# Performance work log

Measured on AMD Instinct MI355X. Metric: run time of the kernel, lower is better.

## Reference

```python
import jax, jax.numpy as jnp
import numpy as np

NEG_SLOPE = 0.2
EPS = 1e-16  # PyG softmax denominator epsilon


def _add_self_loops(src, dst, edge_attr, n):
    # PyG add_self_loops with fill_value='mean': loop edge_attr = mean of
    # incoming edge_attr per target node (0 if no incoming edges).
    cnt = jax.ops.segment_sum(jnp.ones(dst.shape, edge_attr.dtype), dst, n)
    mean_attr = jax.ops.segment_sum(edge_attr, dst, n) / jnp.maximum(cnt, 1.0)[:, None]
    loop = jnp.arange(n)
    return (jnp.concatenate([src, loop]),
            jnp.concatenate([dst, loop]),
            jnp.concatenate([edge_attr, mean_attr], axis=0))


def _gatv2(x, src, dst, eattr, Wl, bl, Wr, br, We, att, bc, n):
    # heads=1, concat=False
    xl = x @ Wl + bl                     # [N, H] source transform
    xr = x @ Wr + br                     # [N, H] target transform
    ee = eattr @ We                      # [E, H]
    m = jax.nn.leaky_relu(xl[src] + xr[dst] + ee, NEG_SLOPE)  # [E, H]
    e = m @ att                          # [E]
    emax = jax.ops.segment_max(e, dst, n)
    emax = jnp.where(jnp.isfinite(emax), emax, 0.0)
    a = jnp.exp(e - emax[dst])
    denom = jax.ops.segment_sum(a, dst, n)
    alpha = a / (denom[dst] + EPS)       # softmax over incoming edges
    out = jax.ops.segment_sum(alpha[:, None] * xl[src], dst, n)  # [N, H]
    return out + bc


def setup_inputs() -> dict:
    key = jax.random.key(0)
    N, E, F_IN, H, E_DIM, OUT = 100000, 1200000, 64, 64, 16, 1
    ks = jax.random.split(key, 20)
    d = {}
    d['x'] = jax.random.normal(ks[0], (N, F_IN), jnp.float32)
    d['edge_index'] = jax.random.randint(ks[1], (2, E), 0, N, jnp.int64)
    d['edge_attr'] = jax.random.normal(ks[2], (E, E_DIM), jnp.float32)
    d['batch'] = jnp.zeros((N,), jnp.int64)
    s = 0.1
    # layer 1: in=F_IN -> H
    d['Wl1'] = jax.random.normal(ks[3], (F_IN, H), jnp.float32) * s
    d['bl1'] = jnp.zeros((H,), jnp.float32)
    d['Wr1'] = jax.random.normal(ks[4], (F_IN, H), jnp.float32) * s
    d['br1'] = jnp.zeros((H,), jnp.float32)
    d['We1'] = jax.random.normal(ks[5], (E_DIM, H), jnp.float32) * s
    d['att1'] = jax.random.normal(ks[6], (H,), jnp.float32) * s
    d['bc1'] = jnp.zeros((H,), jnp.float32)
    # layer 2: H -> H
    d['Wl2'] = jax.random.normal(ks[7], (H, H), jnp.float32) * s
    d['bl2'] = jnp.zeros((H,), jnp.float32)
    d['Wr2'] = jax.random.normal(ks[8], (H, H), jnp.float32) * s
    d['br2'] = jnp.zeros((H,), jnp.float32)
    d['We2'] = jax.random.normal(ks[9], (E_DIM, H), jnp.float32) * s
    d['att2'] = jax.random.normal(ks[10], (H,), jnp.float32) * s
    d['bc2'] = jnp.zeros((H,), jnp.float32)
    # JK(cat) readout: 2*H -> OUT
    d['Wout'] = jax.random.normal(ks[11], (2 * H, OUT), jnp.float32) * s
    d['bout'] = jnp.zeros((OUT,), jnp.float32)
    return d


def reference(x, edge_index, edge_attr, batch,
              Wl1, bl1, Wr1, br1, We1, att1, bc1,
              Wl2, bl2, Wr2, br2, We2, att2, bc2,
              Wout, bout):
    n = x.shape[0]
    src, dst, ea = _add_self_loops(edge_index[0], edge_index[1], edge_attr, n)
    # eval mode: dropout is identity; batch_norms is None
    h1 = jax.nn.relu(_gatv2(x, src, dst, ea, Wl1, bl1, Wr1, br1, We1, att1, bc1, n))
    h2 = jax.nn.relu(_gatv2(h1, src, dst, ea, Wl2, bl2, Wr2, br2, We2, att2, bc2, n))
    h = jnp.concatenate([h1, h2], axis=-1)  # JumpingKnowledge 'cat'
    return h @ Wout + bout                   # [N, out_channels]
```

## Files before the change

### kernel.cpp

```cpp
#include <hip/hip_runtime.h>

constexpr float NEG_SLOPE = 0.2f;
constexpr float EPS = 1e-16f;
constexpr float NEG_INF = -1e30f;

__device__ __forceinline__ unsigned short f2bf(float x) {
    unsigned u = __float_as_uint(x);
    u += 0x7FFF + ((u >> 16) & 1);
    return (unsigned short)(u >> 16);
}
__device__ __forceinline__ float bflo(unsigned u) {
    return __uint_as_float(u << 16);
}
__device__ __forceinline__ float bfhi(unsigned u) {
    return __uint_as_float(u & 0xFFFF0000u);
}
__device__ __forceinline__ unsigned packbf(float a, float b) {
    return (unsigned)f2bf(a) | ((unsigned)f2bf(b) << 16);
}
__device__ __forceinline__ void unpack8(uint4 u, float* o) {
    o[0] = bflo(u.x); o[1] = bfhi(u.x);
    o[2] = bflo(u.y); o[3] = bfhi(u.y);
    o[4] = bflo(u.z); o[5] = bfhi(u.z);
    o[6] = bflo(u.w); o[7] = bfhi(u.w);
}


__global__ void count_k(const int* __restrict__ dst, int* __restrict__ cnt, int E) {
    int i = blockIdx.x * blockDim.x + threadIdx.x;
    if (i < E) atomicAdd(&cnt[dst[i]], 1);
}

__global__ void scan1_k(const int* __restrict__ in, int* __restrict__ out,
                        int* __restrict__ bsum, int n) {
    __shared__ int s[256];
    int tid = threadIdx.x;
    int i = blockIdx.x * 256 + tid;
    int v = (i < n) ? in[i] + 1 : 0;
    s[tid] = v;
    __syncthreads();
    #pragma unroll
    for (int off = 1; off < 256; off <<= 1) {
        int t = (tid >= off) ? s[tid - off] : 0;
        __syncthreads();
        s[tid] += t;
        __syncthreads();
    }
    if (i < n) out[i] = s[tid] - v;
    if (tid == 255) bsum[blockIdx.x] = s[255];
}

__global__ void scan2_k(int* __restrict__ bsum, int nb) {
    __shared__ int s[1024];
    int tid = threadIdx.x;
    int v = (tid < nb) ? bsum[tid] : 0;
    s[tid] = v;
    __syncthreads();
    #pragma unroll
    for (int off = 1; off < 1024; off <<= 1) {
        int t = (tid >= off) ? s[tid - off] : 0;
        __syncthreads();
        s[tid] += t;
        __syncthreads();
    }
    if (tid < nb) bsum[tid] = s[tid] - v;
}

__global__ void scan3_k(int* __restrict__ rowptr, const int* __restrict__ bsum,
                        int n, int M) {
    int i = blockIdx.x * 256 + threadIdx.x;
    if (i < n) rowptr[i] += bsum[blockIdx.x];
    if (i == 0) rowptr[n] = M;
}

__global__ void fill_k(const int* __restrict__ dst,
                       const int* __restrict__ rowptr, int* __restrict__ fill,
                       int* __restrict__ seid, int E) {
    int i = blockIdx.x * blockDim.x + threadIdx.x;
    if (i < E) {
        int d = dst[i];
        int pos = rowptr[d] + atomicAdd(&fill[d], 1);
        seid[pos] = i;
    }
}

__global__ void expand_k(const int* __restrict__ rowptr, int* __restrict__ sdst, int N) {
    int lane = threadIdx.x & 63;
    int v = blockIdx.x * 4 + (threadIdx.x >> 6);
    if (v >= N) return;
    int s = rowptr[v], e = rowptr[v + 1];
    for (int k = s + lane; k < e; k += 64) sdst[k] = v;
}

template <int PERM>
__global__ void build_k(const int* __restrict__ srcA, const float* __restrict__ ea,
                        const int* __restrict__ seid,
                        int* __restrict__ ssrc, unsigned short* __restrict__ eperm_b,
                        int M) {
    int t = blockIdx.x * blockDim.x + threadIdx.x;
    if (t >= M * 2) return;
    int k = t >> 1, c = t & 1;
    int eid = seid[k];
    if (eid < 0) return;
    if (c == 0) ssrc[k] = srcA[eid];
    if (PERM) {
        const float4* s4 = reinterpret_cast<const float4*>(ea) + (size_t)eid * 4 + c * 2;
        float4 a = s4[0], b = s4[1];
        uint4 o;
        o.x = packbf(a.x, a.y);
        o.y = packbf(a.z, a.w);
        o.z = packbf(b.x, b.y);
        o.w = packbf(b.z, b.w);
        reinterpret_cast<uint4*>(eperm_b)[(size_t)k * 2 + c] = o;
    }
}

template <int PERM>
__global__ void mean_k(const float* __restrict__ ea, const int* __restrict__ seid,
                       const int* __restrict__ rowptr,
                       unsigned short* __restrict__ eperm_b, float* __restrict__ mattr,
                       int* __restrict__ ssrc, int N) {
    int t = blockIdx.x * blockDim.x + threadIdx.x;
    if (t >= N * 16) return;
    int v = t >> 4, f = t & 15;
    int s = rowptr[v], sEnd = rowptr[v + 1] - 1;
    float sum = 0.f;
    for (int k = s; k < sEnd; k++) {
        if (PERM) sum += bflo((unsigned)eperm_b[(size_t)k * 16 + f]);
        else      sum += ea[(size_t)seid[k] * 16 + f];
    }
    int c = sEnd - s;
    float mean = sum / (float)(c > 1 ? c : 1);
    if (PERM) eperm_b[(size_t)sEnd * 16 + f] = f2bf(mean);
    else      mattr[(size_t)v * 16 + f] = mean;
    if (f == 0) ssrc[sEnd] = v;
}


__global__ __launch_bounds__(256) void xfrm_k(
        const float* __restrict__ x,
        const float* __restrict__ Wl, const float* __restrict__ bl,
        const float* __restrict__ Wr, const float* __restrict__ br,
        unsigned short* __restrict__ xl_b, unsigned short* __restrict__ xr_b, int N) {
    __shared__ float2 sW[64 * 64];
    for (int i = threadIdx.x; i < 64 * 64; i += 256)
        sW[i] = make_float2(Wl[i], Wr[i]);
    __syncthreads();

    int lane = threadIdx.x & 63;
    int base = __builtin_amdgcn_readfirstlane(
        (blockIdx.x * 4 + (threadIdx.x >> 6)) * 8);
    if (base >= N) return;

    const float4* xb = reinterpret_cast<const float4*>(x);
    int r[8];
    #pragma unroll
    for (int n = 0; n < 8; ++n) r[n] = min(base + n, N - 1) * 16;

    float blh = bl[lane], brh = br[lane];
    float2 acc[8];
    #pragma unroll
    for (int n = 0; n < 8; ++n) acc[n] = make_float2(blh, brh);

    #pragma unroll 4
    for (int d4 = 0; d4 < 16; ++d4) {
        float4 xv[8];
        #pragma unroll
        for (int n = 0; n < 8; ++n) xv[n] = xb[r[n] + d4];
        #pragma unroll
        for (int j = 0; j < 4; ++j) {
            float2 wp = sW[(d4 * 4 + j) * 64 + lane];
            #pragma unroll
            for (int n = 0; n < 8; ++n) {
                float xs = (j == 0) ? xv[n].x : (j == 1) ? xv[n].y
                         : (j == 2) ? xv[n].z : xv[n].w;
                acc[n].x = fmaf(xs, wp.x, acc[n].x);
                acc[n].y = fmaf(xs, wp.y, acc[n].y);
            }
        }
    }

    #pragma unroll
    for (int n = 0; n < 8; ++n) {
        int v = base + n;
        if (v < N) {
            xl_b[(size_t)v * 64 + lane] = f2bf(acc[n].x);
            xr_b[(size_t)v * 64 + lane] = f2bf(acc[n].y);
        }
    }
}


template <int PERM>
__global__ __launch_bounds__(256) void escore_k(
        const unsigned short* __restrict__ xl_b, const unsigned short* __restrict__ xr_b,
        const unsigned short* __restrict__ eperm_b,
        const float* __restrict__ earaw, const int* __restrict__ seid,
        const float* __restrict__ mattr,
        const int* __restrict__ ssrc, const int* __restrict__ sdst,
        const float* __restrict__ We, const float* __restrict__ att,
        float* __restrict__ escr, int M) {
    __shared__ float4 sWe[16 * 16];
    __shared__ float4 sAtt[16];
    int tid = threadIdx.x;
    {
        const float4* We4 = reinterpret_cast<const float4*>(We);
        if (tid < 256) sWe[tid] = We4[tid];
        if (tid < 16) sAtt[tid] = reinterpret_cast<const float4*>(att)[tid];
    }
    __syncthreads();

    int lane = tid & 63;
    int base = (blockIdx.x * 4 + (tid >> 6)) * 128;
    if (base >= M) return;
    int k0 = base + lane;
    int k1 = k0 + 64;
    int k0c = min(k0, M - 1);
    int k1c = min(k1, M - 1);

    int s0 = ssrc[k0c], d0 = sdst[k0c];
    int s1 = ssrc[k1c], d1 = sdst[k1c];

    float ea0[16], ea1[16];
    if (PERM) {
        const uint4* ep4 = reinterpret_cast<const uint4*>(eperm_b);
        uint4 a0 = ep4[(size_t)k0c * 2], a1 = ep4[(size_t)k0c * 2 + 1];
        uint4 b0 = ep4[(size_t)k1c * 2], b1 = ep4[(size_t)k1c * 2 + 1];
        unpack8(a0, ea0); unpack8(a1, ea0 + 8);
        unpack8(b0, ea1); unpack8(b1, ea1 + 8);
    } else {
        int e0 = seid[k0c], e1 = seid[k1c];
        const float4* rp0 = (e0 < 0)
            ? reinterpret_cast<const float4*>(mattr) + (size_t)d0 * 4
            : reinterpret_cast<const float4*>(earaw) + (size_t)e0 * 4;
        const float4* rp1 = (e1 < 0)
            ? reinterpret_cast<const float4*>(mattr) + (size_t)d1 * 4
            : reinterpret_cast<const float4*>(earaw) + (size_t)e1 * 4;
        #pragma unroll
        for (int q = 0; q < 4; q++) {
            float4 a = rp0[q];
            ea0[q * 4 + 0] = a.x; ea0[q * 4 + 1] = a.y;
            ea0[q * 4 + 2] = a.z; ea0[q * 4 + 3] = a.w;
            float4 b = rp1[q];
            ea1[q * 4 + 0] = b.x; ea1[q * 4 + 1] = b.y;
            ea1[q * 4 + 2] = b.z; ea1[q * 4 + 3] = b.w;
        }
    }

    const uint2* xl2 = reinterpret_cast<const uint2*>(xl_b);
    const uint2* xr2 = reinterpret_cast<const uint2*>(xr_b);
    size_t xs0 = (size_t)s0 * 16, xd0 = (size_t)d0 * 16;
    size_t xs1 = (size_t)s1 * 16, xd1 = (size_t)d1 * 16;

    float acc0 = 0.f, acc1 = 0.f;
    #pragma unroll 4
    for (int j = 0; j < 16; ++j) {
        uint2 ux0 = xl2[xs0 + j];
        uint2 ur0 = xr2[xd0 + j];
        uint2 ux1 = xl2[xs1 + j];
        uint2 ur1 = xr2[xd1 + j];
        float4 ee0 = {0.f, 0.f, 0.f, 0.f};
        float4 ee1 = {0.f, 0.f, 0.f, 0.f};
        #pragma unroll
        for (int d = 0; d < 16; ++d) {
            float4 w = sWe[d * 16 + j];
            float a0 = ea0[d], a1 = ea1[d];
            ee0.x = fmaf(a0, w.x, ee0.x);
            ee0.y = fmaf(a0, w.y, ee0.y);
            ee0.z = fmaf(a0, w.z, ee0.z);
            ee0.w = fmaf(a0, w.w, ee0.w);
            ee1.x = fmaf(a1, w.x, ee1.x);
            ee1.y = fmaf(a1, w.y, ee1.y);
            ee1.z = fmaf(a1, w.z, ee1.z);
            ee1.w = fmaf(a1, w.w, ee1.w);
        }
        float4 a4 = sAtt[j];
        float m;
        m = bflo(ux0.x) + bflo(ur0.x) + ee0.x; m = (m > 0.f) ? m : NEG_SLOPE * m; acc0 = fmaf(a4.x, m, acc0);
        m = bfhi(ux0.x) + bfhi(ur0.x) + ee0.y; m = (m > 0.f) ? m : NEG_SLOPE * m; acc0 = fmaf(a4.y, m, acc0);
        m = bflo(ux0.y) + bflo(ur0.y) + ee0.z; m = (m > 0.f) ? m : NEG_SLOPE * m; acc0 = fmaf(a4.z, m, acc0);
        m = bfhi(ux0.y) + bfhi(ur0.y) + ee0.w; m = (m > 0.f) ? m : NEG_SLOPE * m; acc0 = fmaf(a4.w, m, acc0);
        m = bflo(ux1.x) + bflo(ur1.x) + ee1.x; m = (m > 0.f) ? m : NEG_SLOPE * m; acc1 = fmaf(a4.x, m, acc1);
        m = bfhi(ux1.x) + bfhi(ur1.x) + ee1.y; m = (m > 0.f) ? m : NEG_SLOPE * m; acc1 = fmaf(a4.y, m, acc1);
        m = bflo(ux1.y) + bflo(ur1.y) + ee1.z; m = (m > 0.f) ? m : NEG_SLOPE * m; acc1 = fmaf(a4.z, m, acc1);
        m = bfhi(ux1.y) + bfhi(ur1.y) + ee1.w; m = (m > 0.f) ? m : NEG_SLOPE * m; acc1 = fmaf(a4.w, m, acc1);
    }
    if (k0 < M) escr[k0] = acc0;
    if (k1 < M) escr[k1] = acc1;
}


__device__ __forceinline__ float rdlanef(float x, int j) {
    return __int_as_float(__builtin_amdgcn_readlane(__float_as_int(x), j));
}

template <int MODE>
__global__ __launch_bounds__(256) void aggregate_k(
        const unsigned short* __restrict__ xl_b, const float* __restrict__ escr,
        const int* __restrict__ ssrc, const int* __restrict__ rowptr,
        const float* __restrict__ bc,
        float* __restrict__ hout,
        const float* __restrict__ h1, const float* __restrict__ Wout,
        const float* __restrict__ bout, float* __restrict__ out, int N) {
    int lane = threadIdx.x & 63;
    int v = blockIdx.x * 4 + (threadIdx.x >> 6);
    if (v >= N) return;

    int s = rowptr[v], e = rowptr[v + 1];
    int deg = e - s;
    float acc;

    if (deg <= 64) {
        int idx = s + lane;
        bool valid = lane < deg;
        float sc = valid ? escr[idx] : NEG_INF;
        float m = sc;
        #pragma unroll
        for (int off = 32; off; off >>= 1) m = fmaxf(m, __shfl_xor(m, off));
        float t = valid ? __expf(sc - m) : 0.f;
        float dsum = t;
        #pragma unroll
        for (int off = 32; off; off >>= 1) dsum += __shfl_xor(dsum, off);
        float alpha = t / (dsum + EPS);
        int srcn = valid ? ssrc[idx] : 0;

        float a0 = 0.f, a1 = 0.f, a2 = 0.f, a3 = 0.f;
        int j = 0;
        for (; j + 4 <= deg; j += 4) {
            int sj0 = __builtin_amdgcn_readlane(srcn, j);
            int sj1 = __builtin_amdgcn_readlane(srcn, j + 1);
            int sj2 = __builtin_amdgcn_readlane(srcn, j + 2);
            int sj3 = __builtin_amdgcn_readlane(srcn, j + 3);
            float w0 = rdlanef(alpha, j);
            float w1 = rdlanef(alpha, j + 1);
            float w2 = rdlanef(alpha, j + 2);
            float w3 = rdlanef(alpha, j + 3);
            a0 = fmaf(w0, bflo((unsigned)xl_b[(size_t)sj0 * 64 + lane]), a0);
            a1 = fmaf(w1, bflo((unsigned)xl_b[(size_t)sj1 * 64 + lane]), a1);
            a2 = fmaf(w2, bflo((unsigned)xl_b[(size_t)sj2 * 64 + lane]), a2);
            a3 = fmaf(w3, bflo((unsigned)xl_b[(size_t)sj3 * 64 + lane]), a3);
        }
        for (; j < deg; ++j) {
            int sj = __builtin_amdgcn_readlane(srcn, j);
            float wj = rdlanef(alpha, j);
            a0 = fmaf(wj, bflo((unsigned)xl_b[(size_t)sj * 64 + lane]), a0);
        }
        acc = (a0 + a1) + (a2 + a3);
    } else {
        float m = NEG_INF;
        for (int b = s; b < e; b += 64) {
            int idx = b + lane;
            float val = (idx < e) ? escr[idx] : NEG_INF;
            #pragma unroll
            for (int off = 32; off; off >>= 1) val = fmaxf(val, __shfl_xor(val, off));
            m = fmaxf(m, val);
        }
        float denom = 0.f;
        for (int b = s; b < e; b += 64) {
            int idx = b + lane;
            float t = (idx < e) ? __expf(escr[idx] - m) : 0.f;
            #pragma unroll
            for (int off = 32; off; off >>= 1) t += __shfl_xor(t, off);
            denom += t;
        }
        float inv = 1.f / (denom + EPS);
        acc = 0.f;
        for (int b = s; b < e; b += 64) {
            int idx = b + lane;
            float wv = (idx < e) ? __expf(escr[idx] - m) * inv : 0.f;
            int srcn = (idx < e) ? ssrc[idx] : 0;
            int nj = min(64, e - b);
            for (int j = 0; j < nj; ++j) {
                float wk = rdlanef(wv, j);
                int sj = __builtin_amdgcn_readlane(srcn, j);
                acc = fmaf(wk, bflo((unsigned)xl_b[(size_t)sj * 64 + lane]), acc);
            }
        }
    }

    float res = fmaxf(acc + bc[lane], 0.f);

    if (MODE == 0) {
        hout[(size_t)v * 64 + lane] = res;
    } else {
        float part = h1[(size_t)v * 64 + lane] * Wout[lane] + res * Wout[64 + lane];
        #pragma unroll
        for (int off = 32; off; off >>= 1) part += __shfl_xor(part, off);
        if (lane == 0) out[v] = part + bout[0];
    }
}


extern "C" void kernel_launch(void* const* d_in, const int* in_sizes, int n_in,
                              void* d_out, int out_size, void* d_ws, size_t ws_size,
                              hipStream_t stream) {
    const float* x     = (const float*)d_in[0];
    const int*   eidx  = (const int*)d_in[1];
    const float* eattr = (const float*)d_in[2];
    const float* Wl1 = (const float*)d_in[4];
    const float* bl1 = (const float*)d_in[5];
    const float* Wr1 = (const float*)d_in[6];
    const float* br1 = (const float*)d_in[7];
    const float* We1 = (const float*)d_in[8];
    const float* att1 = (const float*)d_in[9];
    const float* bc1 = (const float*)d_in[10];
    const float* Wl2 = (const float*)d_in[11];
    const float* bl2 = (const float*)d_in[12];
    const float* Wr2 = (const float*)d_in[13];
    const float* br2 = (const float*)d_in[14];
    const float* We2 = (const float*)d_in[15];
    const float* att2 = (const float*)d_in[16];
    const float* bc2 = (const float*)d_in[17];
    const float* Wout = (const float*)d_in[18];
    const float* bout = (const float*)d_in[19];

    int N = in_sizes[0] / 64;
    int E = in_sizes[1] / 2;
    int M = E + N;
    const int* srcA = eidx;
    const int* dstA = eidx + E;

    char* w = (char*)d_ws;
    size_t used = 0;
    auto alloc = [&](size_t bytes) {
        char* p = w + used;
        used += (bytes + 255) & ~size_t(255);
        return p;
    };
    int*   cnt    = (int*)alloc((size_t)N * 4);
    int*   fill   = (int*)alloc((size_t)N * 4);
    int*   rowptr = (int*)alloc((size_t)(N + 1) * 4);
    int*   bsum   = (int*)alloc(1024 * 4);
    int*   ssrc   = (int*)alloc((size_t)M * 4);
    int*   sdst   = (int*)alloc((size_t)M * 4);
    int*   seid   = (int*)alloc((size_t)M * 4);
    float* escr   = (float*)alloc((size_t)M * 4);
    float* mattr  = (float*)alloc((size_t)N * 16 * 4);
    unsigned short* xl_b = (unsigned short*)alloc((size_t)N * 64 * 2);
    unsigned short* xr_b = (unsigned short*)alloc((size_t)N * 64 * 2);
    float* h1     = (float*)alloc((size_t)N * 64 * 4);
    size_t eperm_bytes = (size_t)M * 16 * 2;
    bool perm = (used + eperm_bytes) <= ws_size;
    unsigned short* eperm_b = perm ? (unsigned short*)alloc(eperm_bytes) : nullptr;

    hipMemsetAsync(cnt, 0, (size_t)N * 4, stream);
    hipMemsetAsync(fill, 0, (size_t)N * 4, stream);
    hipMemsetAsync(seid, 0xFF, (size_t)M * 4, stream);

    int NB = (N + 255) / 256;
    int nodeBlocks = (N + 3) / 4;
    count_k<<<(E + 255) / 256, 256, 0, stream>>>(dstA, cnt, E);
    scan1_k<<<NB, 256, 0, stream>>>(cnt, rowptr, bsum, N);
    scan2_k<<<1, 1024, 0, stream>>>(bsum, NB);
    scan3_k<<<NB, 256, 0, stream>>>(rowptr, bsum, N, M);
    fill_k<<<(E + 255) / 256, 256, 0, stream>>>(dstA, rowptr, fill, seid, E);
    expand_k<<<nodeBlocks, 256, 0, stream>>>(rowptr, sdst, N);

    if (perm) {
        build_k<1><<<(M * 2 + 255) / 256, 256, 0, stream>>>(srcA, eattr, seid,
                                                            ssrc, eperm_b, M);
        mean_k<1><<<(N * 16 + 255) / 256, 256, 0, stream>>>(
            eattr, seid, rowptr, eperm_b, mattr, ssrc, N);
    } else {
        build_k<0><<<(M * 2 + 255) / 256, 256, 0, stream>>>(srcA, eattr, seid,
                                                            ssrc, nullptr, M);
        mean_k<0><<<(N * 16 + 255) / 256, 256, 0, stream>>>(
            eattr, seid, rowptr, nullptr, mattr, ssrc, N);
    }

    int xfrmBlocks = (N + 31) / 32;
    int slotBlocks = (M + 511) / 512;

    xfrm_k<<<xfrmBlocks, 256, 0, stream>>>(x, Wl1, bl1, Wr1, br1, xl_b, xr_b, N);
    if (perm)
        escore_k<1><<<slotBlocks, 256, 0, stream>>>(xl_b, xr_b, eperm_b, eattr, seid,
                                                    mattr, ssrc, sdst, We1, att1, escr, M);
    else
        escore_k<0><<<slotBlocks, 256, 0, stream>>>(xl_b, xr_b, nullptr, eattr, seid,
                                                    mattr, ssrc, sdst, We1, att1, escr, M);
    aggregate_k<0><<<nodeBlocks, 256, 0, stream>>>(xl_b, escr, ssrc, rowptr, bc1, h1,
                                                   nullptr, nullptr, nullptr, nullptr, N);

    xfrm_k<<<xfrmBlocks, 256, 0, stream>>>(h1, Wl2, bl2, Wr2, br2, xl_b, xr_b, N);
    if (perm)
        escore_k<1><<<slotBlocks, 256, 0, stream>>>(xl_b, xr_b, eperm_b, eattr, seid,
                                                    mattr, ssrc, sdst, We2, att2, escr, M);
    else
        escore_k<0><<<slotBlocks, 256, 0, stream>>>(xl_b, xr_b, nullptr, eattr, seid,
                                                    mattr, ssrc, sdst, We2, att2, escr, M);
    aggregate_k<1><<<nodeBlocks, 256, 0, stream>>>(xl_b, escr, ssrc, rowptr, bc2, nullptr,
                                                   h1, Wout, bout, (float*)d_out, N);
}
```

Measured before the change: 533.0 us.

## Bucket CSR fill by destination, widen escore to 4 slots, store h1 as bf16

The direct atomic CSR fill is replaced by a two-pass scheme. The first pass bins edges into coarse destination buckets using shared-memory counts and writes them to a staging array. The second pass does the per-node atomic placement from that staged order, with an XCD-aware block swizzle so atomics and writes stay more local. The edge-score kernel now handles four slots per lane instead of two, giving more memory-level parallelism at the cost of more registers. h1 is stored in bf16, which halves its write and read traffic but adds rounding error in layer 2 and the readout.

After: 611.9 us. +14.8%, slower.

```diff
diff --git a/kernel.cpp b/kernel.cpp
--- a/kernel.cpp
+++ b/kernel.cpp
@@ -73,15 +73,54 @@
     if (i == 0) rowptr[n] = M;
 }
 
-__global__ void fill_k(const int* __restrict__ dst,
-                       const int* __restrict__ rowptr, int* __restrict__ fill,
-                       int* __restrict__ seid, int E) {
-    int i = blockIdx.x * blockDim.x + threadIdx.x;
-    if (i < E) {
-        int d = dst[i];
-        int pos = rowptr[d] + atomicAdd(&fill[d], 1);
-        seid[pos] = i;
-    }
+
+#define TILE_B 4096
+
+__global__ __launch_bounds__(256) void bucketB_k(
+        const int* __restrict__ dstA, const int* __restrict__ rowptr,
+        int* __restrict__ cursor, int2* __restrict__ stage,
+        int E, int shift, int nbuck) {
+    __shared__ int lcnt[1024];
+    __shared__ int gbase[1024];
+    int tid = threadIdx.x;
+    int base = blockIdx.x * TILE_B;
+    if (base >= E) return;
+    for (int i = tid; i < nbuck; i += 256) lcnt[i] = 0;
+    __syncthreads();
+    int nb = min(TILE_B, E - base);
+    for (int i = tid; i < nb; i += 256) {
+        int d = dstA[base + i];
+        atomicAdd(&lcnt[d >> shift], 1);
+    }
+    __syncthreads();
+    for (int i = tid; i < nbuck; i += 256) {
+        int c = lcnt[i];
+        int g = (c > 0) ? atomicAdd(&cursor[i], c) : 0;
+        gbase[i] = g + rowptr[i << shift] - (i << shift);
+        lcnt[i] = 0;
+    }
+    __syncthreads();
+    for (int i = tid; i < nb; i += 256) {
+        int e = base + i;
+        int d = dstA[e];
+        int b = d >> shift;
+        int off = atomicAdd(&lcnt[b], 1);
+        stage[(size_t)gbase[b] + off] = make_int2(e, d);
+    }
+}
+
+__global__ __launch_bounds__(256) void bucketC_k(
+        const int2* __restrict__ stage, const int* __restrict__ rowptr,
+        int* __restrict__ fill, int* __restrict__ seid, int E, int nblk) {
+    int bid = blockIdx.x;
+    int q = nblk >> 3, r = nblk & 7;
+    int xcd = bid & 7, idx = bid >> 3;
+    int swz = (xcd < r ? xcd * (q + 1) : r * (q + 1) + (xcd - r) * q) + idx;
+    int i = swz * 256 + threadIdx.x;
+    if (i >= E) return;
+    int2 rec = stage[i];
+    int pos = rowptr[rec.y] + atomicAdd(&fill[rec.y], 1);
+    seid[pos] = rec.x;
 }
 
 __global__ void expand_k(const int* __restrict__ rowptr, int* __restrict__ sdst, int N) {
@@ -137,8 +176,9 @@
 }
 
 
+template <int BF>
 __global__ __launch_bounds__(256) void xfrm_k(
-        const float* __restrict__ x,
+        const float* __restrict__ xf, const unsigned short* __restrict__ xb16,
         const float* __restrict__ Wl, const float* __restrict__ bl,
         const float* __restrict__ Wr, const float* __restrict__ br,
         unsigned short* __restrict__ xl_b, unsigned short* __restrict__ xr_b, int N) {
@@ -152,7 +192,8 @@
         (blockIdx.x * 4 + (threadIdx.x >> 6)) * 8);
     if (base >= N) return;
 
-    const float4* xb = reinterpret_cast<const float4*>(x);
+    const float4* xb = reinterpret_cast<const float4*>(xf);
+    const uint2*  xh = reinterpret_cast<const uint2*>(xb16);
     int r[8];
     #pragma unroll
     for (int n = 0; n < 8; ++n) r[n] = min(base + n, N - 1) * 16;
@@ -166,7 +207,14 @@
     for (int d4 = 0; d4 < 16; ++d4) {
         float4 xv[8];
         #pragma unroll
-        for (int n = 0; n < 8; ++n) xv[n] = xb[r[n] + d4];
+        for (int n = 0; n < 8; ++n) {
+            if (BF) {
+                uint2 u = xh[r[n] + d4];
+                xv[n] = make_float4(bflo(u.x), bfhi(u.x), bflo(u.y), bfhi(u.y));
+            } else {
+                xv[n] = xb[r[n] + d4];
+            }
+        }
         #pragma unroll
         for (int j = 0; j < 4; ++j) {
             float2 wp = sW[(d4 * 4 + j) * 64 + lane];
@@ -211,82 +259,87 @@
     __syncthreads();
 
     int lane = tid & 63;
-    int base = (blockIdx.x * 4 + (tid >> 6)) * 128;
+    int base = (blockIdx.x * 4 + (tid >> 6)) * 256;
     if (base >= M) return;
-    int k0 = base + lane;
-    int k1 = k0 + 64;
-    int k0c = min(k0, M - 1);
-    int k1c = min(k1, M - 1);
-
-    int s0 = ssrc[k0c], d0 = sdst[k0c];
-    int s1 = ssrc[k1c], d1 = sdst[k1c];
-
-    float ea0[16], ea1[16];
+
+    int k[4], kk[4];
+    int xs[4], xd[4];
+    #pragma unroll
+    for (int q = 0; q < 4; ++q) {
+        k[q] = base + lane + q * 64;
+        kk[q] = min(k[q], M - 1);
+        xs[q] = ssrc[kk[q]] * 16;
+        xd[q] = sdst[kk[q]] * 16;
+    }
+
+    float ea[4][16];
     if (PERM) {
         const uint4* ep4 = reinterpret_cast<const uint4*>(eperm_b);
-        uint4 a0 = ep4[(size_t)k0c * 2], a1 = ep4[(size_t)k0c * 2 + 1];
-        uint4 b0 = ep4[(size_t)k1c * 2], b1 = ep4[(size_t)k1c * 2 + 1];
-        unpack8(a0, ea0); unpack8(a1, ea0 + 8);
-        unpack8(b0, ea1); unpack8(b1, ea1 + 8);
+        #pragma unroll
+        for (int q = 0; q < 4; ++q) {
+            uint4 a = ep4[(size_t)kk[q] * 2], b = ep4[(size_t)kk[q] * 2 + 1];
+            unpack8(a, ea[q]); unpack8(b, ea[q] + 8);
+        }
     } else {
-        int e0 = seid[k0c], e1 = seid[k1c];
-        const float4* rp0 = (e0 < 0)
-            ? reinterpret_cast<const float4*>(mattr) + (size_t)d0 * 4
-            : reinterpret_cast<const float4*>(earaw) + (size_t)e0 * 4;
-        const float4* rp1 = (e1 < 0)
-            ? reinterpret_cast<const float4*>(mattr) + (size_t)d1 * 4
-            : reinterpret_cast<const float4*>(earaw) + (size_t)e1 * 4;
-        #pragma unroll
-        for (int q = 0; q < 4; q++) {
-            float4 a = rp0[q];
-            ea0[q * 4 + 0] = a.x; ea0[q * 4 + 1] = a.y;
-            ea0[q * 4 + 2] = a.z; ea0[q * 4 + 3] = a.w;
-            float4 b = rp1[q];
-            ea1[q * 4 + 0] = b.x; ea1[q * 4 + 1] = b.y;
-            ea1[q * 4 + 2] = b.z; ea1[q * 4 + 3] = b.w;
+        #pragma unroll
+        for (int q = 0; q < 4; ++q) {
+            int eid = seid[kk[q]];
+            const float4* rp = (eid < 0)
+                ? reinterpret_cast<const float4*>(mattr) + (size_t)(xd[q] / 16) * 4
+                : reinterpret_cast<const float4*>(earaw) + (size_t)eid * 4;
+            #pragma unroll
+            for (int u = 0; u < 4; u++) {
+                float4 a = rp[u];
+                ea[q][u * 4 + 0] = a.x; ea[q][u * 4 + 1] = a.y;
+                ea[q][u * 4 + 2] = a.z; ea[q][u * 4 + 3] = a.w;
+            }
         }
     }
 
     const uint2* xl2 = reinterpret_cast<const uint2*>(xl_b);
     const uint2* xr2 = reinterpret_cast<const uint2*>(xr_b);
-    size_t xs0 = (size_t)s0 * 16, xd0 = (size_t)d0 * 16;
-    size_t xs1 = (size_t)s1 * 16, xd1 = (size_t)d1 * 16;
-
-    float acc0 = 0.f, acc1 = 0.f;
-    #pragma unroll 4
+
+    float acc[4] = {0.f, 0.f, 0.f, 0.f};
+    #pragma unroll 2
     for (int j = 0; j < 16; ++j) {
-        uint2 ux0 = xl2[xs0 + j];
-        uint2 ur0 = xr2[xd0 + j];
-        uint2 ux1 = xl2[xs1 + j];
-        uint2 ur1 = xr2[xd1 + j];
-        float4 ee0 = {0.f, 0.f, 0.f, 0.f};
-        float4 ee1 = {0.f, 0.f, 0.f, 0.f};
+        uint2 ux[4], ur[4];
+        #pragma unroll
+        for (int q = 0; q < 4; ++q) {
+            ux[q] = xl2[(size_t)xs[q] + j];
+            ur[q] = xr2[(size_t)xd[q] + j];
+        }
+        float4 ee[4];
+        #pragma unroll
+        for (int q = 0; q < 4; ++q) ee[q] = make_float4(0.f, 0.f, 0.f, 0.f);
         #pragma unroll
         for (int d = 0; d < 16; ++d) {
             float4 w = sWe[d * 16 + j];
-            float a0 = ea0[d], a1 = ea1[d];
-            ee0.x = fmaf(a0, w.x, ee0.x);
-            ee0.y = fmaf(a0, w.y, ee0.y);
-            ee0.z = fmaf(a0, w.z, ee0.z);
-            ee0.w = fmaf(a0, w.w, ee0.w);
-            ee1.x = fmaf(a1, w.x, ee1.x);
-            ee1.y = fmaf(a1, w.y, ee1.y);
-            ee1.z = fmaf(a1, w.z, ee1.z);
-            ee1.w = fmaf(a1, w.w, ee1.w);
+            #pragma unroll
+            for (int q = 0; q < 4; ++q) {
+                float a = ea[q][d];
+                ee[q].x = fmaf(a, w.x, ee[q].x);
+                ee[q].y = fmaf(a, w.y, ee[q].y);
+                ee[q].z = fmaf(a, w.z, ee[q].z);
+                ee[q].w = fmaf(a, w.w, ee[q].w);
+            }
         }
         float4 a4 = sAtt[j];
-        float m;
-        m = bflo(ux0.x) + bflo(ur0.x) + ee0.x; m = (m > 0.f) ? m : NEG_SLOPE * m; acc0 = fmaf(a4.x, m, acc0);
-        m = bfhi(ux0.x) + bfhi(ur0.x) + ee0.y; m = (m > 0.f) ? m : NEG_SLOPE * m; acc0 = fmaf(a4.y, m, acc0);
-        m = bflo(ux0.y) + bflo(ur0.y) + ee0.z; m = (m > 0.f) ? m : NEG_SLOPE * m; acc0 = fmaf(a4.z, m, acc0);
-        m = bfhi(ux0.y) + bfhi(ur0.y) + ee0.w; m = (m > 0.f) ? m : NEG_SLOPE * m; acc0 = fmaf(a4.w, m, acc0);
-        m = bflo(ux1.x) + bflo(ur1.x) + ee1.x; m = (m > 0.f) ? m : NEG_SLOPE * m; acc1 = fmaf(a4.x, m, acc1);
-        m = bfhi(ux1.x) + bfhi(ur1.x) + ee1.y; m = (m > 0.f) ? m : NEG_SLOPE * m; acc1 = fmaf(a4.y, m, acc1);
-        m = bflo(ux1.y) + bflo(ur1.y) + ee1.z; m = (m > 0.f) ? m : NEG_SLOPE * m; acc1 = fmaf(a4.z, m, acc1);
-        m = bfhi(ux1.y) + bfhi(ur1.y) + ee1.w; m = (m > 0.f) ? m : NEG_SLOPE * m; acc1 = fmaf(a4.w, m, acc1);
-    }
-    if (k0 < M) escr[k0] = acc0;
-    if (k1 < M) escr[k1] = acc1;
+        #pragma unroll
+        for (int q = 0; q < 4; ++q) {
+            float m;
+            m = bflo(ux[q].x) + bflo(ur[q].x) + ee[q].x;
+            m = (m > 0.f) ? m : NEG_SLOPE * m; acc[q] = fmaf(a4.x, m, acc[q]);
+            m = bfhi(ux[q].x) + bfhi(ur[q].x) + ee[q].y;
+            m = (m > 0.f) ? m : NEG_SLOPE * m; acc[q] = fmaf(a4.y, m, acc[q]);
+            m = bflo(ux[q].y) + bflo(ur[q].y) + ee[q].z;
+            m = (m > 0.f) ? m : NEG_SLOPE * m; acc[q] = fmaf(a4.z, m, acc[q]);
+            m = bfhi(ux[q].y) + bfhi(ur[q].y) + ee[q].w;
+            m = (m > 0.f) ? m : NEG_SLOPE * m; acc[q] = fmaf(a4.w, m, acc[q]);
+        }
+    }
+    #pragma unroll
+    for (int q = 0; q < 4; ++q)
+        if (k[q] < M) escr[k[q]] = acc[q];
 }
 
 
@@ -299,8 +352,8 @@
         const unsigned short* __restrict__ xl_b, const float* __restrict__ escr,
         const int* __restrict__ ssrc, const int* __restrict__ rowptr,
         const float* __restrict__ bc,
-        float* __restrict__ hout,
-        const float* __restrict__ h1, const float* __restrict__ Wout,
+        unsigned short* __restrict__ hout_b,
+        const unsigned short* __restrict__ h1_b, const float* __restrict__ Wout,
         const float* __restrict__ bout, float* __restrict__ out, int N) {
     int lane = threadIdx.x & 63;
     int v = blockIdx.x * 4 + (threadIdx.x >> 6);
@@ -381,9 +434,10 @@
     float res = fmaxf(acc + bc[lane], 0.f);
 
     if (MODE == 0) {
-        hout[(size_t)v * 64 + lane] = res;
+        hout_b[(size_t)v * 64 + lane] = f2bf(res);
     } else {
-        float part = h1[(size_t)v * 64 + lane] * Wout[lane] + res * Wout[64 + lane];
+        float part = bflo((unsigned)h1_b[(size_t)v * 64 + lane]) * Wout[lane]
+                   + res * Wout[64 + lane];
         #pragma unroll
         for (int off = 32; off; off >>= 1) part += __shfl_xor(part, off);
         if (lane == 0) out[v] = part + bout[0];
@@ -420,6 +474,10 @@
     const int* srcA = eidx;
     const int* dstA = eidx + E;
 
+    int shift = 10;
+    while ((((N - 1) >> shift) + 1) > 1024) shift++;
+    int nbuck = ((N - 1) >> shift) + 1;
+
     char* w = (char*)d_ws;
     size_t used = 0;
     auto alloc = [&](size_t bytes) {
@@ -431,20 +489,23 @@
     int*   fill   = (int*)alloc((size_t)N * 4);
     int*   rowptr = (int*)alloc((size_t)(N + 1) * 4);
     int*   bsum   = (int*)alloc(1024 * 4);
+    int*   cursor = (int*)alloc(1024 * 4);
     int*   ssrc   = (int*)alloc((size_t)M * 4);
     int*   sdst   = (int*)alloc((size_t)M * 4);
     int*   seid   = (int*)alloc((size_t)M * 4);
+    int2*  stage  = (int2*)alloc((size_t)E * 8);
     float* escr   = (float*)alloc((size_t)M * 4);
     float* mattr  = (float*)alloc((size_t)N * 16 * 4);
     unsigned short* xl_b = (unsigned short*)alloc((size_t)N * 64 * 2);
     unsigned short* xr_b = (unsigned short*)alloc((size_t)N * 64 * 2);
-    float* h1     = (float*)alloc((size_t)N * 64 * 4);
+    unsigned short* h1_b = (unsigned short*)alloc((size_t)N * 64 * 2);
     size_t eperm_bytes = (size_t)M * 16 * 2;
     bool perm = (used + eperm_bytes) <= ws_size;
     unsigned short* eperm_b = perm ? (unsigned short*)alloc(eperm_bytes) : nullptr;
 
     hipMemsetAsync(cnt, 0, (size_t)N * 4, stream);
     hipMemsetAsync(fill, 0, (size_t)N * 4, stream);
+    hipMemsetAsync(cursor, 0, 1024 * 4, stream);
     hipMemsetAsync(seid, 0xFF, (size_t)M * 4, stream);
 
     int NB = (N + 255) / 256;
@@ -453,7 +514,12 @@
     scan1_k<<<NB, 256, 0, stream>>>(cnt, rowptr, bsum, N);
     scan2_k<<<1, 1024, 0, stream>>>(bsum, NB);
     scan3_k<<<NB, 256, 0, stream>>>(rowptr, bsum, N, M);
-    fill_k<<<(E + 255) / 256, 256, 0, stream>>>(dstA, rowptr, fill, seid, E);
+
+    int blkB = (E + TILE_B - 1) / TILE_B;
+    bucketB_k<<<blkB, 256, 0, stream>>>(dstA, rowptr, cursor, stage, E, shift, nbuck);
+    int blkC = (E + 255) / 256;
+    bucketC_k<<<blkC, 256, 0, stream>>>(stage, rowptr, fill, seid, E, blkC);
+
     expand_k<<<nodeBlocks, 256, 0, stream>>>(rowptr, sdst, N);
 
     if (perm) {
@@ -469,19 +535,21 @@
     }
 
     int xfrmBlocks = (N + 31) / 32;
-    int slotBlocks = (M + 511) / 512;
-
-    xfrm_k<<<xfrmBlocks, 256, 0, stream>>>(x, Wl1, bl1, Wr1, br1, xl_b, xr_b, N);
+    int slotBlocks = (M + 1023) / 1024;
+
+    xfrm_k<0><<<xfrmBlocks, 256, 0, stream>>>(x, nullptr, Wl1, bl1, Wr1, br1,
+                                              xl_b, xr_b, N);
     if (perm)
         escore_k<1><<<slotBlocks, 256, 0, stream>>>(xl_b, xr_b, eperm_b, eattr, seid,
                                                     mattr, ssrc, sdst, We1, att1, escr, M);
     else
         escore_k<0><<<slotBlocks, 256, 0, stream>>>(xl_b, xr_b, nullptr, eattr, seid,
                                                     mattr, ssrc, sdst, We1, att1, escr, M);
-    aggregate_k<0><<<nodeBlocks, 256, 0, stream>>>(xl_b, escr, ssrc, rowptr, bc1, h1,
+    aggregate_k<0><<<nodeBlocks, 256, 0, stream>>>(xl_b, escr, ssrc, rowptr, bc1, h1_b,
                                                    nullptr, nullptr, nullptr, nullptr, N);
 
-    xfrm_k<<<xfrmBlocks, 256, 0, stream>>>(h1, Wl2, bl2, Wr2, br2, xl_b, xr_b, N);
+    xfrm_k<1><<<xfrmBlocks, 256, 0, stream>>>(nullptr, h1_b, Wl2, bl2, Wr2, br2,
+                                              xl_b, xr_b, N);
     if (perm)
         escore_k<1><<<slotBlocks, 256, 0, stream>>>(xl_b, xr_b, eperm_b, eattr, seid,
                                                     mattr, ssrc, sdst, We2, att2, escr, M);
@@ -489,5 +557,5 @@
         escore_k<0><<<slotBlocks, 256, 0, stream>>>(xl_b, xr_b, nullptr, eattr, seid,
                                                     mattr, ssrc, sdst, We2, att2, escr, M);
     aggregate_k<1><<<nodeBlocks, 256, 0, stream>>>(xl_b, escr, ssrc, rowptr, bc2, nullptr,
-                                                   h1, Wout, bout, (float*)d_out, N);
-}
+                                                   h1_b, Wout, bout, (float*)d_out, N);
+}
```
